# Performance work log

Hardware: AMD Instinct MI355X
Metric: run time of the kernel (lower is better)

The kernel has to match this reference:

```python
import jax, jax.numpy as jnp
import numpy as np

B, S, D_MODEL, D_FF = 4, 2048, 1024, 4096


def setup_inputs() -> dict:
    key = jax.random.key(0)
    ks = jax.random.split(key, 8)
    return {
        "x": jax.random.normal(ks[0], (B, S, D_MODEL), dtype=jnp.float32),
        "W1": jax.random.normal(ks[1], (D_MODEL, D_FF), dtype=jnp.float32) * (1.0 / np.sqrt(D_MODEL)),
        "b1": jnp.zeros((D_FF,), dtype=jnp.float32),
        "quantum_phases": jax.random.normal(ks[2], (D_FF,), dtype=jnp.float32) * (2.0 * np.pi),
        "quantum_weights_real": jax.random.normal(ks[3], (D_FF,), dtype=jnp.float32) * 0.1,
        "quantum_weights_imag": jax.random.normal(ks[4], (D_FF,), dtype=jnp.float32) * 0.1,
        "W2": jax.random.normal(ks[5], (D_FF, D_MODEL), dtype=jnp.float32) * (1.0 / np.sqrt(D_FF)),
        "b2": jnp.zeros((D_MODEL,), dtype=jnp.float32),
    }


def _quantum_transform(hidden, theta, w_real, w_imag):
    # hidden: [B,S,d_ff]; theta/w_real/w_imag: [d_ff] broadcast over channels
    imag = w_imag * jnp.sin(theta + hidden * 0.1)
    quantum_phase = jnp.cos(theta) * w_real + jnp.sin(theta) * w_imag  # [d_ff]
    return hidden + quantum_phase * imag * 0.1


def reference(x, W1, b1, quantum_phases, quantum_weights_real, quantum_weights_imag, W2, b2):
    hidden = jnp.einsum("bsd,df->bsf", x, W1) + b1  # [B,S,d_ff]
    q = _quantum_transform(hidden, quantum_phases, quantum_weights_real, quantum_weights_imag)
    act = jax.nn.relu(q)  # dropout is identity in eval mode
    return jnp.einsum("bsf,fd->bsd", act, W2) + b2
```

## Files before the change

kernel.cpp:

```cpp
#include <hip/hip_runtime.h>

typedef __bf16 bf16x8 __attribute__((ext_vector_type(8)));
typedef short  s16x8  __attribute__((ext_vector_type(8)));
typedef float  f32x4  __attribute__((ext_vector_type(4)));

#define DEVINL __device__ __forceinline__

DEVINL unsigned short f2bf(float f) {
  unsigned int u = __builtin_bit_cast(unsigned int, f);
  u += 0x7fffu + ((u >> 16) & 1u);
  return (unsigned short)(u >> 16);
}

DEVINL void async16(const void* g, void* l) {
  __builtin_amdgcn_global_load_lds(
      (const __attribute__((address_space(1))) unsigned int*)g,
      (__attribute__((address_space(3))) unsigned int*)l, 16, 0, 0);
}


__global__ __launch_bounds__(256) void prep(
    const float* __restrict__ x, const float* __restrict__ W1,
    const float* __restrict__ W2, const float* __restrict__ theta,
    const float* __restrict__ wre, const float* __restrict__ wim,
    unsigned short* __restrict__ xb, unsigned short* __restrict__ w1t,
    unsigned short* __restrict__ w2t, float* __restrict__ c1) {
  __shared__ unsigned short tile[32][33];
  const int b = blockIdx.x;
  const int tid = threadIdx.x;
  if (b < 1024) {
    int i = b * 256 + tid;
#pragma unroll
    for (int k = 0; k < 8; ++k, i += 262144) {
      float4 v = ((const float4*)x)[i];
      ushort4 o;
      o.x = f2bf(v.x); o.y = f2bf(v.y); o.z = f2bf(v.z); o.w = f2bf(v.w);
      ((ushort4*)xb)[i] = o;
    }
  } else if (b < 5120) {
    int bb = b - 1024;
    int bc = (bb & 127) * 32, br = (bb >> 7) * 32;
    int tx = tid & 31, ty = tid >> 5;
#pragma unroll
    for (int i = 0; i < 32; i += 8)
      tile[ty + i][tx] = f2bf(W1[(size_t)(br + ty + i) * 4096 + (bc + tx)]);
    __syncthreads();
#pragma unroll
    for (int i = 0; i < 32; i += 8)
      w1t[(size_t)(bc + ty + i) * 1024 + (br + tx)] = tile[tx][ty + i];
  } else if (b < 9216) {
    int bb = b - 5120;
    int bc = (bb & 31) * 32, br = (bb >> 5) * 32;
    int tx = tid & 31, ty = tid >> 5;
#pragma unroll
    for (int i = 0; i < 32; i += 8)
      tile[ty + i][tx] = f2bf(W2[(size_t)(br + ty + i) * 1024 + (bc + tx)]);
    __syncthreads();
#pragma unroll
    for (int i = 0; i < 32; i += 8)
      w2t[(size_t)(bc + ty + i) * 4096 + (br + tx)] = tile[tx][ty + i];
  } else {
    int i = (b - 9216) * 256 + tid;
    float t = theta[i];
    c1[i] = (cosf(t) * wre[i] + sinf(t) * wim[i]) * wim[i] * 0.1f;
  }
}


__global__ __launch_bounds__(512, 1) void gemm1k(
    const unsigned short* __restrict__ A,
    const unsigned short* __restrict__ Bt,
    const float* __restrict__ bias,
    const float* __restrict__ theta,
    const float* __restrict__ c1,
    unsigned short* __restrict__ Cout) {
  constexpr int K = 1024, N = 4096, NT = 16, REPS = 2;
  constexpr int WROWS = 128, M_REP = 8, MH = 4;
  constexpr int ABYTES = 32768, AH = 16384, AL = 2;
  constexpr int BUFSZ = 65536;
  constexpr int nTilesN = 8;

  __shared__ __align__(16) char lds[2 * BUFSZ + 16384];

  int nwg = gridDim.x;
  int wg = blockIdx.x;
  int sw = (wg & 7) * (nwg >> 3) + (wg >> 3);
  int rowBase = (sw / nTilesN) * 256;
  int colBase = (sw % nTilesN) * 512;

  const int t = threadIdx.x;
  const int lane = t & 63;
  const int wid = t >> 6;
  const int wr = wid >> 2, wc = wid & 3;
  const int lr = lane & 15;
  const int lg = lane >> 4;
  const int r7 = lane & 7;

  const int srow = t >> 3;
  const int scolB = ((t & 7) * 16) ^ ((srow & 7) << 4);
  const unsigned short* aSrcB = A  + (size_t)(rowBase + srow) * K + (scolB >> 1);
  const unsigned short* bSrcB = Bt + (size_t)(colBase + srow) * K + (scolB >> 1);

  const int aRd = (wr * WROWS + lr) * 128 + ((lg ^ r7) << 4);
  const int bRd = ABYTES + (wc * 64 + lr) * 128 + ((lg ^ r7) << 4);

#define STAGE_AU(S, U, P) do {                                              \
    _Pragma("unroll") for (int j = 0; j < AL; ++j)                          \
      async16(aSrcB + ((size_t)((U) * WROWS + j * 64) * K + (size_t)(S) * 64),\
              &lds[(P) * BUFSZ + (U) * AH + j * 8192 + t * 16]);            \
  } while (0)
#define STAGE_BU(SRC, S, U, P) do {                                         \
    _Pragma("unroll") for (int j = 0; j < 2; ++j)                           \
      async16((SRC) + ((size_t)((U) * 128 + j * 64) * K + (size_t)(S) * 64),\
              &lds[(P) * BUFSZ + ABYTES + (U) * 16384 + j * 8192 + t * 16]);\
  } while (0)
#define LOAD_A(MHh, P)                                                      \
  _Pragma("unroll") for (int mi = 0; mi < MH; ++mi)                         \
  _Pragma("unroll") for (int ks = 0; ks < 2; ++ks)                          \
    a[mi][ks] = __builtin_bit_cast(bf16x8, *(const s16x8*)&lds[             \
        (P) * BUFSZ + ((aRd + ((MHh) * MH + mi) * 2048) ^ (ks << 6))])
#define LOAD_B(NHh, P)                                                      \
  _Pragma("unroll") for (int nn = 0; nn < 2; ++nn)                          \
  _Pragma("unroll") for (int ks = 0; ks < 2; ++ks)                          \
    b[(NHh) * 2 + nn][ks] = __builtin_bit_cast(bf16x8, *(const s16x8*)&lds[ \
        (P) * BUFSZ + ((bRd + ((NHh) * 2 + nn) * 2048) ^ (ks << 6))])
#define QUAD(MHh, NHh)                                                      \
  __builtin_amdgcn_s_setprio(1);                                            \
  _Pragma("unroll") for (int mi = 0; mi < MH; ++mi)                         \
  _Pragma("unroll") for (int nn = 0; nn < 2; ++nn)                          \
  _Pragma("unroll") for (int ks = 0; ks < 2; ++ks)                          \
    acc[(MHh) * MH + mi][(NHh) * 2 + nn] =                                  \
        __builtin_amdgcn_mfma_f32_16x16x32_bf16(                            \
            a[mi][ks], b[(NHh) * 2 + nn][ks],                               \
            acc[(MHh) * MH + mi][(NHh) * 2 + nn], 0, 0, 0);                 \
  __builtin_amdgcn_s_setprio(0)
#define BAR() __builtin_amdgcn_s_barrier()
#define LG0() asm volatile("s_waitcnt lgkmcnt(0)" ::: "memory")
#define TILE(T, P) do {                                                     \
    LOAD_A(0, P); LOAD_B(0, P);                                             \
    if ((T) + 1 < NT) STAGE_AU((T) + 1, 0, (P) ^ 1);                        \
    asm volatile("s_waitcnt lgkmcnt(8)" ::: "memory");                      \
    BAR(); LG0(); QUAD(0, 0); BAR();                                        \
    LOAD_B(1, P);                                                           \
    if ((T) + 1 < NT) STAGE_AU((T) + 1, 1, (P) ^ 1);                        \
    BAR(); LG0(); QUAD(0, 1); BAR();                                        \
    LOAD_A(1, P);                                                           \
    if ((T) + 2 < NT) STAGE_BU(bSrcR, (T) + 2, 0, P);                       \
    BAR(); LG0(); QUAD(1, 1); BAR();                                        \
    if ((T) + 2 < NT) STAGE_BU(bSrcR, (T) + 2, 1, P);                       \
    BAR(); QUAD(1, 0);                                                      \
    if ((T) + 2 < NT) {                                                     \
      asm volatile("s_waitcnt vmcnt(4)" ::: "memory");                      \
    } else if ((T) + 1 < NT) {                                              \
      asm volatile("s_waitcnt vmcnt(0)" ::: "memory");                      \
    }                                                                       \
    BAR();                                                                  \
  } while (0)

  STAGE_AU(0, 0, 0); STAGE_AU(0, 1, 0);
  STAGE_BU(bSrcB, 0, 0, 0); STAGE_BU(bSrcB, 0, 1, 0);
  STAGE_BU(bSrcB, 1, 0, 1); STAGE_BU(bSrcB, 1, 1, 1);
  asm volatile("s_waitcnt vmcnt(4)" ::: "memory");
  BAR();

  for (int rep = 0; rep < REPS; ++rep) {
    const unsigned short* bSrcR = bSrcB + (size_t)rep * 256 * K;
    f32x4 acc[M_REP][4] = {};
    bf16x8 a[MH][2], b[4][2];

    for (int T = 0; T < NT; T += 2) {
      TILE(T, 0);
      TILE(T + 1, 1);
    }

    if (rep + 1 < REPS) {
      const unsigned short* bSrcN = bSrcB + (size_t)(rep + 1) * 256 * K;
      STAGE_AU(0, 0, 0); STAGE_AU(0, 1, 0);
      STAGE_BU(bSrcN, 0, 0, 0); STAGE_BU(bSrcN, 0, 1, 0);
      STAGE_BU(bSrcN, 1, 0, 1); STAGE_BU(bSrcN, 1, 1, 1);
    }

    const int colR = colBase + rep * 256;
    const int ocol0 = colR + wc * 64 + lr;
    float bvv[4], thv[4], ccv[4];
#pragma unroll
    for (int ni = 0; ni < 4; ++ni) {
      int n = ocol0 + ni * 16;
      bvv[ni] = bias[n]; thv[ni] = theta[n]; ccv[ni] = c1[n];
    }
    const int SB = 2 * BUFSZ + wid * 2048;
    const size_t growB = (size_t)(rowBase + wr * WROWS) * N;
    const int rd = lane >> 3;
    const int bo = (lane & 7) * 16;
#pragma unroll
    for (int mi = 0; mi < M_REP; ++mi) {
#pragma unroll
      for (int ni = 0; ni < 4; ++ni) {
#pragma unroll
        for (int r = 0; r < 4; ++r) {
          int row16 = lg * 4 + r;
          float h = acc[mi][ni][r] + bvv[ni];
          float q = h + ccv[ni] * __sinf(thv[ni] + 0.1f * h);
          unsigned short v = f2bf(fmaxf(q, 0.f));
          int ad = SB + row16 * 128 +
                   (((ni * 16 + lr) * 2) ^ ((row16 & 7) << 4));
          *(unsigned short*)&lds[ad] = v;
        }
      }
      s16x8 w0 = *(const s16x8*)&lds[SB + rd * 128 + (bo ^ ((rd & 7) << 4))];
      s16x8 w1 = *(const s16x8*)&lds[SB + (rd + 8) * 128 +
                                     (bo ^ ((rd & 7) << 4))];
      unsigned short* dst = Cout + growB + (size_t)(mi * 16 + rd) * N +
                            colR + wc * 64 + (lane & 7) * 8;
      *(s16x8*)dst = w0;
      *(s16x8*)(dst + (size_t)8 * N) = w1;
    }

    if (rep + 1 < REPS) {
      asm volatile("s_waitcnt vmcnt(0)" ::: "memory");
      BAR();
    }
  }
#undef TILE
#undef QUAD
#undef LOAD_A
#undef LOAD_B
#undef STAGE_AU
#undef STAGE_BU
#undef BAR
#undef LG0
}


__global__ __launch_bounds__(512, 1) void gemm2k(
    const unsigned short* __restrict__ A,
    const unsigned short* __restrict__ Bt,
    const float* __restrict__ bias,
    float* __restrict__ Cout) {
  constexpr int K = 4096, N = 1024, NT = 64;
  constexpr int WROWS = 64, M_REP = 4, MH = 2;
  constexpr int ABYTES = 16384, AH = 8192, AL = 1;
  constexpr int BUFSZ = 49152;
  constexpr int nTilesN = 4;

  __shared__ __align__(16) char lds[2 * BUFSZ + 32768];

  int nwg = gridDim.x;
  int wg = blockIdx.x;
  int sw = (wg & 7) * (nwg >> 3) + (wg >> 3);
  int rowBase = (sw / nTilesN) * 128;
  int colBase = (sw % nTilesN) * 256;

  const int t = threadIdx.x;
  const int lane = t & 63;
  const int wid = t >> 6;
  const int wr = wid >> 2, wc = wid & 3;
  const int lr = lane & 15;
  const int lg = lane >> 4;
  const int r7 = lane & 7;

  const int srow = t >> 3;
  const int scolB = ((t & 7) * 16) ^ ((srow & 7) << 4);
  const unsigned short* aSrcB = A  + (size_t)(rowBase + srow) * K + (scolB >> 1);
  const unsigned short* bSrcB = Bt + (size_t)(colBase + srow) * K + (scolB >> 1);

  const int aRd = (wr * WROWS + lr) * 128 + ((lg ^ r7) << 4);
  const int bRd = ABYTES + (wc * 64 + lr) * 128 + ((lg ^ r7) << 4);

  f32x4 acc[M_REP][4] = {};
  bf16x8 a[MH][2], b[4][2];

#define STAGE_AU(S, U, P)                                                   \
  async16(aSrcB + ((size_t)((U) * 64) * K + (size_t)(S) * 64),              \
          &lds[(P) * BUFSZ + (U) * AH + t * 16])
#define STAGE_BU(S, U, P) do {                                              \
    _Pragma("unroll") for (int j = 0; j < 2; ++j)                           \
      async16(bSrcB + ((size_t)((U) * 128 + j * 64) * K + (size_t)(S) * 64),\
              &lds[(P) * BUFSZ + ABYTES + (U) * 16384 + j * 8192 + t * 16]);\
  } while (0)
#define LOAD_A(MHh, P)                                                      \
  _Pragma("unroll") for (int mi = 0; mi < MH; ++mi)                         \
  _Pragma("unroll") for (int ks = 0; ks < 2; ++ks)                          \
    a[mi][ks] = __builtin_bit_cast(bf16x8, *(const s16x8*)&lds[             \
        (P) * BUFSZ + ((aRd + ((MHh) * MH + mi) * 2048) ^ (ks << 6))])
#define LOAD_B(NHh, P)                                                      \
  _Pragma("unroll") for (int nn = 0; nn < 2; ++nn)                          \
  _Pragma("unroll") for (int ks = 0; ks < 2; ++ks)                          \
    b[(NHh) * 2 + nn][ks] = __builtin_bit_cast(bf16x8, *(const s16x8*)&lds[ \
        (P) * BUFSZ + ((bRd + ((NHh) * 2 + nn) * 2048) ^ (ks << 6))])
#define QUAD(MHh, NHh)                                                      \
  __builtin_amdgcn_s_setprio(1);                                            \
  _Pragma("unroll") for (int mi = 0; mi < MH; ++mi)                         \
  _Pragma("unroll") for (int nn = 0; nn < 2; ++nn)                          \
  _Pragma("unroll") for (int ks = 0; ks < 2; ++ks)                          \
    acc[(MHh) * MH + mi][(NHh) * 2 + nn] =                                  \
        __builtin_amdgcn_mfma_f32_16x16x32_bf16(                            \
            a[mi][ks], b[(NHh) * 2 + nn][ks],                               \
            acc[(MHh) * MH + mi][(NHh) * 2 + nn], 0, 0, 0);                 \
  __builtin_amdgcn_s_setprio(0)
#define BAR() __builtin_amdgcn_s_barrier()
#define LG0() asm volatile("s_waitcnt lgkmcnt(0)" ::: "memory")
#define TILE(T, P) do {                                                     \
    LOAD_A(0, P); LOAD_B(0, P);                                             \
    if ((T) + 1 < NT) STAGE_AU((T) + 1, 0, (P) ^ 1);                        \
    BAR(); LG0(); QUAD(0, 0); BAR();                                        \
    LOAD_B(1, P);                                                           \
    if ((T) + 1 < NT) STAGE_AU((T) + 1, 1, (P) ^ 1);                        \
    BAR(); LG0(); QUAD(0, 1); BAR();                                        \
    LOAD_A(1, P);                                                           \
    if ((T) + 2 < NT) STAGE_BU((T) + 2, 0, P);                              \
    BAR(); LG0(); QUAD(1, 1); BAR();                                        \
    if ((T) + 2 < NT) STAGE_BU((T) + 2, 1, P);                              \
    BAR(); QUAD(1, 0);                                                      \
    if ((T) + 2 < NT) {                                                     \
      asm volatile("s_waitcnt vmcnt(4)" ::: "memory");                      \
    } else if ((T) + 1 < NT) {                                              \
      asm volatile("s_waitcnt vmcnt(0)" ::: "memory");                      \
    }                                                                       \
    BAR();                                                                  \
  } while (0)

  STAGE_AU(0, 0, 0); STAGE_AU(0, 1, 0);
  STAGE_BU(0, 0, 0); STAGE_BU(0, 1, 0);
  STAGE_BU(1, 0, 1); STAGE_BU(1, 1, 1);
  asm volatile("s_waitcnt vmcnt(4)" ::: "memory");
  BAR();

  for (int T = 0; T < NT; T += 2) {
    TILE(T, 0);
    TILE(T + 1, 1);
  }
#undef TILE
#undef QUAD
#undef LOAD_A
#undef LOAD_B
#undef STAGE_AU
#undef STAGE_BU
#undef BAR

  const int ocol0 = colBase + wc * 64 + lr;
  float bvv[4];
#pragma unroll
  for (int ni = 0; ni < 4; ++ni) bvv[ni] = bias[ocol0 + ni * 16];
  const int SB = 2 * BUFSZ + wid * 4096;
  const int orowB = rowBase + wr * WROWS;
  const int rd = lane >> 3;
  const int bo = (lane & 7) * 16;
#pragma unroll
  for (int mi = 0; mi < M_REP; ++mi) {
#pragma unroll
    for (int ni = 0; ni < 4; ++ni) {
#pragma unroll
      for (int r = 0; r < 4; ++r) {
        int row16 = lg * 4 + r;
        int ad = SB + row16 * 256 +
                 (((ni * 16 + lr) * 4) ^ ((row16 & 7) << 4));
        *(float*)&lds[ad] = acc[mi][ni][r] + bvv[ni];
      }
    }
    asm volatile("s_waitcnt lgkmcnt(0)" ::: "memory");
    f32x4 v00 = *(const f32x4*)&lds[SB + rd * 256 + (bo ^ ((rd & 7) << 4))];
    f32x4 v01 = *(const f32x4*)&lds[SB + rd * 256 +
                                    ((bo + 128) ^ ((rd & 7) << 4))];
    f32x4 v10 = *(const f32x4*)&lds[SB + (rd + 8) * 256 +
                                    (bo ^ ((rd & 7) << 4))];
    f32x4 v11 = *(const f32x4*)&lds[SB + (rd + 8) * 256 +
                                    ((bo + 128) ^ ((rd & 7) << 4))];
    float* dst0 = Cout + (size_t)(orowB + mi * 16 + rd) * N +
                  colBase + wc * 64 + (lane & 7) * 4;
    *(f32x4*)dst0 = v00;
    *(f32x4*)(dst0 + 32) = v01;
    float* dst1 = dst0 + (size_t)8 * N;
    *(f32x4*)dst1 = v10;
    *(f32x4*)(dst1 + 32) = v11;
    asm volatile("s_waitcnt lgkmcnt(0)" ::: "memory");
  }
}


extern "C" void kernel_launch(void* const* d_in, const int* in_sizes, int n_in,
                              void* d_out, int out_size, void* d_ws,
                              size_t ws_size, hipStream_t stream) {
  const float* x     = (const float*)d_in[0];
  const float* W1    = (const float*)d_in[1];
  const float* b1    = (const float*)d_in[2];
  const float* theta = (const float*)d_in[3];
  const float* qwr   = (const float*)d_in[4];
  const float* qwi   = (const float*)d_in[5];
  const float* W2    = (const float*)d_in[6];
  const float* b2    = (const float*)d_in[7];
  float* out = (float*)d_out;

  const int DF = 4096;
  size_t need = ((size_t)96 << 20) + DF * sizeof(float);
  if (ws_size < need) return;

  char* ws = (char*)d_ws;
  unsigned short* xb   = (unsigned short*)ws;
  unsigned short* w1t  = (unsigned short*)(ws + ((size_t)16 << 20));
  unsigned short* w2t  = (unsigned short*)(ws + ((size_t)24 << 20));
  unsigned short* actb = (unsigned short*)(ws + ((size_t)32 << 20));
  float* c1 = (float*)(ws + ((size_t)96 << 20));

  prep<<<9232, 256, 0, stream>>>(x, W1, W2, theta, qwr, qwi,
                                 xb, w1t, w2t, c1);
  gemm1k<<<256, 512, 0, stream>>>(xb, w1t, b1, theta, c1, actb);
  gemm2k<<<256, 512, 0, stream>>>(actb, w2t, b2, out);
}
```

Measured before the change: 154.7 us.

## Cut per-tile barriers in GEMM1 main loop and batch async staging

Restructures the software-pipelined K loop so that each tile issues both A-stage and both B-stage async global-to-LDS loads together. The MFMA quads run back to back with only two barriers per tile instead of about eight. The end-of-rep wait is relaxed from vmcnt(0) to vmcnt(16), so the epilogue's global stores need not drain before the next rep starts. Removing synchronisation points gives the scheduler longer uninterrupted MFMA streams. The cost is tighter reliance on the LDS buffer hazards being ordered correctly and on the vmcnt accounting covering the prefetched loads.

```diff
diff --git a/kernel.cpp b/kernel.cpp
--- a/kernel.cpp
+++ b/kernel.cpp
@@ -136,22 +136,29 @@
   __builtin_amdgcn_s_setprio(0)
 #define BAR() __builtin_amdgcn_s_barrier()
 #define LG0() asm volatile("s_waitcnt lgkmcnt(0)" ::: "memory")
-#define TILE(T, P) do {                                                     \
+#define WIN(T, P) do {                                                      \
+                                                                \
     LOAD_A(0, P); LOAD_B(0, P);                                             \
-    if ((T) + 1 < NT) STAGE_AU((T) + 1, 0, (P) ^ 1);                        \
-    asm volatile("s_waitcnt lgkmcnt(8)" ::: "memory");                      \
-    BAR(); LG0(); QUAD(0, 0); BAR();                                        \
+    if ((T) + 1 < NT) {                                                     \
+      STAGE_AU((T) + 1, 0, (P) ^ 1);                                        \
+      STAGE_AU((T) + 1, 1, (P) ^ 1);                                        \
+    }                                                                       \
+    QUAD(0, 0);                                                             \
     LOAD_B(1, P);                                                           \
-    if ((T) + 1 < NT) STAGE_AU((T) + 1, 1, (P) ^ 1);                        \
-    BAR(); LG0(); QUAD(0, 1); BAR();                                        \
+    QUAD(0, 1);                                                             \
+    LG0(); BAR();                                                           \
+                                                                \
     LOAD_A(1, P);                                                           \
-    if ((T) + 2 < NT) STAGE_BU(bSrcR, (T) + 2, 0, P);                       \
-    BAR(); LG0(); QUAD(1, 1); BAR();                                        \
-    if ((T) + 2 < NT) STAGE_BU(bSrcR, (T) + 2, 1, P);                       \
-    BAR(); QUAD(1, 0);                                                      \
     if ((T) + 2 < NT) {                                                     \
+      STAGE_BU(bSrcR, (T) + 2, 0, P);                                       \
+      STAGE_BU(bSrcR, (T) + 2, 1, P);                                       \
+    }                                                                       \
+    QUAD(1, 0);                                                             \
+    QUAD(1, 1);                                                             \
+    LG0();                                                                  \
+    if ((T) < NT - 2) {                                                     \
       asm volatile("s_waitcnt vmcnt(4)" ::: "memory");                      \
-    } else if ((T) + 1 < NT) {                                              \
+    } else if ((T) == NT - 2) {                                             \
       asm volatile("s_waitcnt vmcnt(0)" ::: "memory");                      \
     }                                                                       \
     BAR();                                                                  \
@@ -169,8 +176,8 @@
     bf16x8 a[MH][2], b[4][2];
 
     for (int T = 0; T < NT; T += 2) {
-      TILE(T, 0);
-      TILE(T + 1, 1);
+      WIN(T, 0);
+      WIN(T + 1, 1);
     }
 
     if (rep + 1 < REPS) {
@@ -217,11 +224,11 @@
     }
 
     if (rep + 1 < REPS) {
-      asm volatile("s_waitcnt vmcnt(0)" ::: "memory");
+      asm volatile("s_waitcnt vmcnt(16)" ::: "memory");
       BAR();
     }
   }
-#undef TILE
+#undef WIN
 #undef QUAD
 #undef LOAD_A
 #undef LOAD_B
```

New measurement: 152.8 us. No clear change (-1.2%).

## Restructure first GEMM main loop into two-window double-buffered schedule with A prefetch

Applied to the files above, without the earlier changes.

Replaces the four-barrier-per-tile ping-pong schedule in the first GEMM kernel with two half-tile windows per tile. Each window issues its LDS fragment reads and MFMA quads. The A fragments for the next tile are prefetched into a separate register set (a0/a1) while the current tile's second half computes. Global-to-LDS staging of both A and B is moved to a single point per tile, two tiles ahead, which cuts barriers and keeps the MFMA pipe fed. The cost is more VGPRs for the extra A fragments, a full vmcnt(0) wait each tile, and new buffer reuse timing that must stay race-free.

```diff
diff --git a/kernel.cpp b/kernel.cpp
--- a/kernel.cpp
+++ b/kernel.cpp
@@ -114,69 +114,82 @@
       async16((SRC) + ((size_t)((U) * 128 + j * 64) * K + (size_t)(S) * 64),\
               &lds[(P) * BUFSZ + ABYTES + (U) * 16384 + j * 8192 + t * 16]);\
   } while (0)
-#define LOAD_A(MHh, P)                                                      \
+#define LOAD_A0(P)                                                          \
   _Pragma("unroll") for (int mi = 0; mi < MH; ++mi)                         \
   _Pragma("unroll") for (int ks = 0; ks < 2; ++ks)                          \
-    a[mi][ks] = __builtin_bit_cast(bf16x8, *(const s16x8*)&lds[             \
-        (P) * BUFSZ + ((aRd + ((MHh) * MH + mi) * 2048) ^ (ks << 6))])
+    a0[mi][ks] = __builtin_bit_cast(bf16x8, *(const s16x8*)&lds[            \
+        (P) * BUFSZ + ((aRd + mi * 2048) ^ (ks << 6))])
+#define LOAD_A1(P)                                                          \
+  _Pragma("unroll") for (int mi = 0; mi < MH; ++mi)                         \
+  _Pragma("unroll") for (int ks = 0; ks < 2; ++ks)                          \
+    a1[mi][ks] = __builtin_bit_cast(bf16x8, *(const s16x8*)&lds[            \
+        (P) * BUFSZ + ((aRd + (MH + mi) * 2048) ^ (ks << 6))])
 #define LOAD_B(NHh, P)                                                      \
   _Pragma("unroll") for (int nn = 0; nn < 2; ++nn)                          \
   _Pragma("unroll") for (int ks = 0; ks < 2; ++ks)                          \
     b[(NHh) * 2 + nn][ks] = __builtin_bit_cast(bf16x8, *(const s16x8*)&lds[ \
         (P) * BUFSZ + ((bRd + ((NHh) * 2 + nn) * 2048) ^ (ks << 6))])
-#define QUAD(MHh, NHh)                                                      \
+#define QUAD(AF, MOFF, NHh)                                                 \
   __builtin_amdgcn_s_setprio(1);                                            \
   _Pragma("unroll") for (int mi = 0; mi < MH; ++mi)                         \
   _Pragma("unroll") for (int nn = 0; nn < 2; ++nn)                          \
   _Pragma("unroll") for (int ks = 0; ks < 2; ++ks)                          \
-    acc[(MHh) * MH + mi][(NHh) * 2 + nn] =                                  \
+    acc[(MOFF) + mi][(NHh) * 2 + nn] =                                      \
         __builtin_amdgcn_mfma_f32_16x16x32_bf16(                            \
-            a[mi][ks], b[(NHh) * 2 + nn][ks],                               \
-            acc[(MHh) * MH + mi][(NHh) * 2 + nn], 0, 0, 0);                 \
+            AF[mi][ks], b[(NHh) * 2 + nn][ks],                              \
+            acc[(MOFF) + mi][(NHh) * 2 + nn], 0, 0, 0);                     \
   __builtin_amdgcn_s_setprio(0)
 #define BAR() __builtin_amdgcn_s_barrier()
 #define LG0() asm volatile("s_waitcnt lgkmcnt(0)" ::: "memory")
-#define TILE(T, P) do {                                                     \
-    LOAD_A(0, P); LOAD_B(0, P);                                             \
-    if ((T) + 1 < NT) STAGE_AU((T) + 1, 0, (P) ^ 1);                        \
-    asm volatile("s_waitcnt lgkmcnt(8)" ::: "memory");                      \
-    BAR(); LG0(); QUAD(0, 0); BAR();                                        \
-    LOAD_B(1, P);                                                           \
-    if ((T) + 1 < NT) STAGE_AU((T) + 1, 1, (P) ^ 1);                        \
-    BAR(); LG0(); QUAD(0, 1); BAR();                                        \
-    LOAD_A(1, P);                                                           \
-    if ((T) + 2 < NT) STAGE_BU(bSrcR, (T) + 2, 0, P);                       \
-    BAR(); LG0(); QUAD(1, 1); BAR();                                        \
-    if ((T) + 2 < NT) STAGE_BU(bSrcR, (T) + 2, 1, P);                       \
-    BAR(); QUAD(1, 0);                                                      \
+#define WIN_A(T, P) do {                                                    \
+    LOAD_B(0, P); LOAD_B(1, P);                                             \
+    LOAD_A1(P);                                                             \
+    QUAD(a0, 0, 0);                                                         \
+    QUAD(a0, 0, 1);                                                         \
+    LG0();                                                                  \
+    asm volatile("s_waitcnt vmcnt(0)" ::: "memory");                        \
+    BAR();                                                                  \
+  } while (0)
+#define WIN_B(T, P) do {                                                    \
     if ((T) + 2 < NT) {                                                     \
-      asm volatile("s_waitcnt vmcnt(4)" ::: "memory");                      \
-    } else if ((T) + 1 < NT) {                                              \
-      asm volatile("s_waitcnt vmcnt(0)" ::: "memory");                      \
+      STAGE_AU((T) + 2, 0, P); STAGE_AU((T) + 2, 1, P);                     \
+      STAGE_BU(bSrcR, (T) + 2, 0, P); STAGE_BU(bSrcR, (T) + 2, 1, P);       \
     }                                                                       \
-    BAR();                                                                  \
-  } while (0)
-
-  STAGE_AU(0, 0, 0); STAGE_AU(0, 1, 0);
-  STAGE_BU(bSrcB, 0, 0, 0); STAGE_BU(bSrcB, 0, 1, 0);
-  STAGE_BU(bSrcB, 1, 0, 1); STAGE_BU(bSrcB, 1, 1, 1);
-  asm volatile("s_waitcnt vmcnt(4)" ::: "memory");
+    if ((T) + 1 < NT) LOAD_A0((P) ^ 1);                                     \
+    QUAD(a1, MH, 0);                                                        \
+    QUAD(a1, MH, 1);                                                        \
+    LG0(); BAR();                                                           \
+  } while (0)
+
+  {
+    const unsigned short* bSrcR = bSrcB;
+    STAGE_AU(0, 0, 0); STAGE_AU(0, 1, 0);
+    STAGE_BU(bSrcR, 0, 0, 0); STAGE_BU(bSrcR, 0, 1, 0);
+    STAGE_AU(1, 0, 1); STAGE_AU(1, 1, 1);
+    STAGE_BU(bSrcR, 1, 0, 1); STAGE_BU(bSrcR, 1, 1, 1);
+  }
+  asm volatile("s_waitcnt vmcnt(8)" ::: "memory");
   BAR();
 
   for (int rep = 0; rep < REPS; ++rep) {
     const unsigned short* bSrcR = bSrcB + (size_t)rep * 256 * K;
     f32x4 acc[M_REP][4] = {};
-    bf16x8 a[MH][2], b[4][2];
+    bf16x8 a0[MH][2], a1[MH][2], b[4][2];
+
+    LOAD_A0(0);
 
     for (int T = 0; T < NT; T += 2) {
-      TILE(T, 0);
-      TILE(T + 1, 1);
+      WIN_A(T, 0);
+      WIN_B(T, 0);
+      WIN_A(T + 1, 1);
+      WIN_B(T + 1, 1);
     }
 
     if (rep + 1 < REPS) {
       const unsigned short* bSrcN = bSrcB + (size_t)(rep + 1) * 256 * K;
       STAGE_AU(0, 0, 0); STAGE_AU(0, 1, 0);
       STAGE_BU(bSrcN, 0, 0, 0); STAGE_BU(bSrcN, 0, 1, 0);
+      STAGE_AU(1, 0, 1); STAGE_AU(1, 1, 1);
       STAGE_BU(bSrcN, 1, 0, 1); STAGE_BU(bSrcN, 1, 1, 1);
     }
 
@@ -217,13 +230,15 @@
     }
 
     if (rep + 1 < REPS) {
-      asm volatile("s_waitcnt vmcnt(0)" ::: "memory");
+      asm volatile("s_waitcnt vmcnt(16)" ::: "memory");
       BAR();
     }
   }
-#undef TILE
+#undef WIN_A
+#undef WIN_B
 #undef QUAD
-#undef LOAD_A
+#undef LOAD_A0
+#undef LOAD_A1
 #undef LOAD_B
 #undef STAGE_AU
 #undef STAGE_BU
```

Measured after the change: 209.4 us. 35.3% more time.
